# Kernel tuning notes

Measured on AMD Instinct MI355X. Metric: run time of the kernel, lower is better.

The kernel has to match this reference:

```python
import jax, jax.numpy as jnp
import numpy as np

N = 50000   # nodes
E = 800000  # edges (before self-loops)
IN = 256    # in_dim
H = 4       # heads
C = 64      # out_dim per head
NEG_SLOPE = 0.2
BN_EPS = 1e-5


def setup_inputs() -> dict:
    key = jax.random.key(0)
    ks = jax.random.split(key, 6)
    feature = jax.random.normal(ks[0], (N, IN), jnp.float32)
    edge_index = jax.random.randint(ks[1], (2, E), 0, N, dtype=jnp.int64)
    W = jax.random.normal(ks[2], (IN, H * C), jnp.float32) * 0.05
    att_src = jax.random.normal(ks[3], (H, C), jnp.float32) * 0.1
    att_dst = jax.random.normal(ks[4], (H, C), jnp.float32) * 0.1
    bias = jnp.zeros((H * C,), jnp.float32)
    gamma = jnp.ones((H * C,), jnp.float32)
    beta = jnp.zeros((H * C,), jnp.float32)
    return {"feature": feature, "edge_index": edge_index, "W": W,
            "att_src": att_src, "att_dst": att_dst, "bias": bias,
            "gamma": gamma, "beta": beta}


def reference(feature, edge_index, W, att_src, att_dst, bias, gamma, beta):
    n = feature.shape[0]
    # linear projection -> [N, H, C]
    x = (feature @ W).reshape(n, H, C)
    # per-node attention logits [N, H]
    a_src = jnp.einsum('nhc,hc->nh', x, att_src)
    a_dst = jnp.einsum('nhc,hc->nh', x, att_dst)
    # add self loops (PyG GATConv default)
    loop = jnp.arange(n, dtype=edge_index.dtype)
    src = jnp.concatenate([edge_index[0], loop])
    dst = jnp.concatenate([edge_index[1], loop])
    # edge attention scores [E+N, H]
    e = jax.nn.leaky_relu(a_src[src] + a_dst[dst], NEG_SLOPE)
    # segment softmax over incoming edges of each dst node
    m = jax.ops.segment_max(e, dst, num_segments=n)
    ex = jnp.exp(e - m[dst])
    denom = jax.ops.segment_sum(ex, dst, num_segments=n)
    alpha = ex / denom[dst]                       # [E+N, H]
    # weighted message aggregation -> [N, H, C]
    msg = x[src] * alpha[:, :, None]
    out = jax.ops.segment_sum(msg, dst, num_segments=n)
    h = out.reshape(n, H * C) + bias
    # batchnorm over nodes (training-mode batch statistics)
    mu = jnp.mean(h, axis=0)
    var = jnp.var(h, axis=0)
    h = (h - mu) * jax.lax.rsqrt(var + BN_EPS) * gamma + beta
    # ELU activation
    h = jax.nn.elu(h)
    # residual (in_dim == out_dim * num_heads)
    return feature + h
```

## Files before the change

### kernel.cpp

```cpp
#include <hip/hip_runtime.h>

#define N_NODES 50000
#define N_EDGES 800000
#define NEG_SLOPE 0.2f
#define BN_EPS  1e-5f
#define LOG2E   1.44269504088896f

#define CHUNKS 256
#define EDGES_PER_CHUNK 3125
#define NCOARSE 1024
#define NBUCKET 782
#define GEMM_BLOCKS 782

typedef short bf16x8 __attribute__((ext_vector_type(8)));
typedef float floatx4 __attribute__((ext_vector_type(4)));

__device__ inline ushort f2bf(float f) {
    union { float f; unsigned u; } v; v.f = f;
    unsigned r = v.u + 0x7fff + ((v.u >> 16) & 1);
    return (ushort)(r >> 16);
}
__device__ inline float bf2f(ushort h) {
    union { unsigned u; float f; } v; v.u = ((unsigned)h) << 16;
    return v.f;
}

__global__ __launch_bounds__(256) void count_wt_kernel(const int* __restrict__ ei,
                                                       const float* __restrict__ W,
                                                       int* __restrict__ counts,
                                                       ushort* __restrict__ Wtb,
                                                       float* __restrict__ bnacc)
{
    __shared__ int hist[NCOARSE];
    const int t = threadIdx.x;
    const int b = blockIdx.x;
    if (b < CHUNKS) {
        for (int j = t; j < NCOARSE; j += 256) hist[j] = 0;
        __syncthreads();
        const int e0 = b * EDGES_PER_CHUNK;
        for (int e = e0 + t; e < e0 + EDGES_PER_CHUNK; e += 256)
            atomicAdd(&hist[ei[N_EDGES + e] >> 6], 1);
        __syncthreads();
        for (int j = t; j < NCOARSE; j += 256)
            counts[j * CHUNKS + b] = hist[j];
    } else {
        const int n = b - CHUNKS;
        Wtb[n * 256 + t] = f2bf(W[t * 256 + n]);
        if (n < 16) bnacc[n * 256 + t] = 0.f;
    }
}

__global__ __launch_bounds__(256) void sscan1_kernel(int* __restrict__ counts,
                                                     int* __restrict__ blocksum)
{
    __shared__ int sm[256];
    const int t = threadIdx.x;
    const int i = blockIdx.x * 256 + t;
    const int v = counts[i];
    sm[t] = v;
    __syncthreads();
#pragma unroll
    for (int off = 1; off < 256; off <<= 1) {
        const int u = (t >= off) ? sm[t - off] : 0;
        __syncthreads();
        sm[t] += u;
        __syncthreads();
    }
    counts[i] = sm[t] - v;
    if (t == 255) blocksum[blockIdx.x] = sm[255];
}

#define LDSTRIDE 40
__global__ __launch_bounds__(256) void scatter_gemm_kernel(const int* __restrict__ ei,
                                                           const int* __restrict__ counts,
                                                           const int* __restrict__ blocksum,
                                                           int* __restrict__ blockbase,
                                                           uint* __restrict__ tmp,
                                                           const float* __restrict__ A,
                                                           const ushort* __restrict__ Bt,
                                                           const float* __restrict__ att_src,
                                                           const float* __restrict__ att_dst,
                                                           ushort* __restrict__ Xb,
                                                           float* __restrict__ s,
                                                           float* __restrict__ d)
{
    __shared__ __align__(16) char smem[25600];
    const int tid = threadIdx.x;

    if (blockIdx.x < CHUNKS) {
        int* sm     = (int*)smem;
        int* bbase  = sm + 256;
        int* cursor = bbase + NCOARSE;
        const int t = tid;
        const int blk = blockIdx.x;

        int v[4], loc[4], tot = 0;
#pragma unroll
        for (int j = 0; j < 4; ++j) {
            v[j] = blocksum[t * 4 + j];
            loc[j] = tot;
            tot += v[j];
        }
        sm[t] = tot;
        __syncthreads();
#pragma unroll
        for (int off = 1; off < 256; off <<= 1) {
            const int u = (t >= off) ? sm[t - off] : 0;
            __syncthreads();
            sm[t] += u;
            __syncthreads();
        }
        const int base = sm[t] - tot;
#pragma unroll
        for (int j = 0; j < 4; ++j) bbase[t * 4 + j] = base + loc[j];
        if (blk == 0) {
#pragma unroll
            for (int j = 0; j < 4; ++j) blockbase[t * 4 + j] = base + loc[j];
        }
        __syncthreads();

        for (int u = t; u < NCOARSE; u += 256)
            cursor[u] = counts[u * CHUNKS + blk] + bbase[u];
        __syncthreads();
        const int e0 = blk * EDGES_PER_CHUNK;
        for (int e = e0 + t; e < e0 + EDGES_PER_CHUNK; e += 256) {
            const int src = ei[e];
            const int dst = ei[N_EDGES + e];
            const int pos = atomicAdd(&cursor[dst >> 6], 1);
            tmp[pos] = ((uint)src << 6) | (uint)(dst & 63);
        }
        return;
    }

    ushort* As = (ushort*)smem;
    ushort* Bs = As + 64 * LDSTRIDE;
    const int lane = tid & 63;
    const int wid = tid >> 6;
    const int row0 = (blockIdx.x - CHUNKS) * 64;
    const int quad = lane >> 4;
    const int l16  = lane & 15;

    floatx4 acc[4][4] = {};

    const int lr = tid >> 2;
    const int lk = (tid & 3) * 8;

    for (int k0 = 0; k0 < 256; k0 += 32) {
        {
            const int grow = row0 + lr;
            union { ushort u[8]; ulonglong2 v; } cv;
            if (grow < N_NODES) {
                const float4 f0 = *(const float4*)(A + (size_t)grow * 256 + k0 + lk);
                const float4 f1 = *(const float4*)(A + (size_t)grow * 256 + k0 + lk + 4);
                cv.u[0] = f2bf(f0.x); cv.u[1] = f2bf(f0.y);
                cv.u[2] = f2bf(f0.z); cv.u[3] = f2bf(f0.w);
                cv.u[4] = f2bf(f1.x); cv.u[5] = f2bf(f1.y);
                cv.u[6] = f2bf(f1.z); cv.u[7] = f2bf(f1.w);
            } else {
                cv.v = ulonglong2{0ull, 0ull};
            }
            *(ulonglong2*)(As + lr * LDSTRIDE + lk) = cv.v;
        }
#pragma unroll
        for (int r = 0; r < 4; ++r) {
            const int row = lr + r * 64;
            const ulonglong2 bv = *(const ulonglong2*)(Bt + (size_t)row * 256 + k0 + lk);
            *(ulonglong2*)(Bs + row * LDSTRIDE + lk) = bv;
        }
        __syncthreads();
        bf16x8 afrag[4], bfrag[4];
#pragma unroll
        for (int mi = 0; mi < 4; ++mi)
            afrag[mi] = *(const bf16x8*)(As + (mi * 16 + l16) * LDSTRIDE + quad * 8);
#pragma unroll
        for (int ni = 0; ni < 4; ++ni)
            bfrag[ni] = *(const bf16x8*)(Bs + (wid * 64 + ni * 16 + l16) * LDSTRIDE + quad * 8);
#pragma unroll
        for (int mi = 0; mi < 4; ++mi)
#pragma unroll
            for (int ni = 0; ni < 4; ++ni)
                acc[mi][ni] = __builtin_amdgcn_mfma_f32_16x16x32_bf16(afrag[mi], bfrag[ni], acc[mi][ni], 0, 0, 0);
        __syncthreads();
    }

    const int head = wid;
    float as_l[4], ad_l[4];
#pragma unroll
    for (int ni = 0; ni < 4; ++ni) {
        const int ch = head * 64 + ni * 16 + l16;
        as_l[ni] = att_src[ch];
        ad_l[ni] = att_dst[ch];
    }
#pragma unroll
    for (int mi = 0; mi < 4; ++mi) {
#pragma unroll
        for (int r = 0; r < 4; ++r) {
            const int grow = row0 + mi * 16 + quad * 4 + r;
            const bool ok = grow < N_NODES;
            float vs = 0.f, vd = 0.f;
            ushort4 o;
#pragma unroll
            for (int ni = 0; ni < 4; ++ni) {
                const float v = acc[mi][ni][r];
                vs += v * as_l[ni];
                vd += v * ad_l[ni];
                ((ushort*)&o)[ni] = f2bf(v);
            }
            if (ok)
                *(ushort4*)(Xb + (size_t)grow * 256 + head * 64 + l16 * 4) = o;
#pragma unroll
            for (int m = 8; m >= 1; m >>= 1) {
                vs += __shfl_xor(vs, m);
                vd += __shfl_xor(vd, m);
            }
            if (l16 == 0 && ok) {
                s[grow * 4 + head] = vs * LOG2E;
                d[grow * 4 + head] = vd * LOG2E;
            }
        }
    }
}

__global__ __launch_bounds__(256) void bucket_build_kernel(const uint* __restrict__ tmp,
                                                           const int* __restrict__ blockbase,
                                                           int* __restrict__ offsets,
                                                           int* __restrict__ csr_src)
{
    __shared__ int hist[64];
    __shared__ int sbuf[64];
    __shared__ int cursor[64];
    const int t = threadIdx.x;
    const int b = blockIdx.x;
    const int start = blockbase[b];
    const int end   = blockbase[b + 1];
    if (t < 64) hist[t] = 0;
    __syncthreads();
    for (int e = start + t; e < end; e += 256)
        atomicAdd(&hist[tmp[e] & 63], 1);
    __syncthreads();
    const int v = (t < 64) ? hist[t] : 0;
    if (t < 64) sbuf[t] = v;
    __syncthreads();
#pragma unroll
    for (int off = 1; off < 64; off <<= 1) {
        int u = 0;
        if (t < 64 && t >= off) u = sbuf[t - off];
        __syncthreads();
        if (t < 64) sbuf[t] += u;
        __syncthreads();
    }
    if (t < 64) {
        const int excl = start + sbuf[t] - v;
        cursor[t] = excl;
        const int node = b * 64 + t;
        if (node < N_NODES) offsets[node] = excl;
    }
    if (b == 0 && t == 0) offsets[N_NODES] = N_EDGES;
    __syncthreads();
    for (int e = start + t; e < end; e += 256) {
        const uint p = tmp[e];
        const int pos = atomicAdd(&cursor[p & 63], 1);
        csr_src[pos] = (int)(p >> 6);
    }
}

__global__ __launch_bounds__(256) void aggregate_kernel(const ushort* __restrict__ xb,
                                                        const float* __restrict__ s,
                                                        const float* __restrict__ d,
                                                        const int* __restrict__ offsets,
                                                        const int* __restrict__ csr_src,
                                                        ushort* __restrict__ hagg,
                                                        float* __restrict__ bnacc)
{
    __shared__ float bsum[4][256];
    __shared__ float bsq[4][256];
    const int wid = threadIdx.x >> 6;
    const int lane = threadIdx.x & 63;
    const int n = blockIdx.x * 4 + wid;
    const int h = lane >> 4;
    const float dn = d[n * 4 + h];
    const float sn = s[n * 4 + h];
    const ushort4 xr = *(const ushort4*)(xb + (size_t)n * 256 + lane * 4);
    float eself = sn + dn;
    eself = eself >= 0.f ? eself : NEG_SLOPE * eself;
    const float pself = exp2f(eself);
    float den = pself;
    float a0 = pself * bf2f(xr.x), a1 = pself * bf2f(xr.y);
    float a2 = pself * bf2f(xr.z), a3 = pself * bf2f(xr.w);
    const int e0 = __builtin_amdgcn_readfirstlane(offsets[n]);
    const int e1 = __builtin_amdgcn_readfirstlane(offsets[n + 1]);
    for (int e = e0; e < e1; e += 8) {
        int si[8];
        float lg[8];
        ushort4 xv[8];
#pragma unroll
        for (int j = 0; j < 8; ++j) {
            const int idx = e + j;
            const int idx2 = idx < e1 ? idx : e1 - 1;
            si[j] = __builtin_amdgcn_readfirstlane(csr_src[idx2]);
        }
#pragma unroll
        for (int j = 0; j < 8; ++j) lg[j] = s[si[j] * 4 + h] + dn;
#pragma unroll
        for (int j = 0; j < 8; ++j)
            xv[j] = *(const ushort4*)(xb + (size_t)si[j] * 256 + lane * 4);
#pragma unroll
        for (int j = 0; j < 8; ++j) {
            float l = (e + j < e1) ? lg[j] : -1e30f;
            l = l >= 0.f ? l : NEG_SLOPE * l;
            const float p = exp2f(l);
            den += p;
            a0 += p * bf2f(xv[j].x);
            a1 += p * bf2f(xv[j].y);
            a2 += p * bf2f(xv[j].z);
            a3 += p * bf2f(xv[j].w);
        }
    }
    const float inv = 1.0f / den;
    ushort4 o;
    o.x = f2bf(a0 * inv); o.y = f2bf(a1 * inv);
    o.z = f2bf(a2 * inv); o.w = f2bf(a3 * inv);
    *(ushort4*)(hagg + (size_t)n * 256 + lane * 4) = o;

    const float v0 = bf2f(o.x), v1 = bf2f(o.y), v2 = bf2f(o.z), v3 = bf2f(o.w);
    *(float4*)&bsum[wid][lane * 4] = float4{v0, v1, v2, v3};
    *(float4*)&bsq[wid][lane * 4]  = float4{v0 * v0, v1 * v1, v2 * v2, v3 * v3};
    __syncthreads();
    const int c = threadIdx.x;
    const float smv = bsum[0][c] + bsum[1][c] + bsum[2][c] + bsum[3][c];
    const float sqv = bsq[0][c]  + bsq[1][c]  + bsq[2][c]  + bsq[3][c];
    const int rep = (blockIdx.x & 7) * 256 + c;
    atomicAdd(&bnacc[rep], smv);
    atomicAdd(&bnacc[2048 + rep], sqv);
}

__global__ __launch_bounds__(256) void finalize_kernel(const float* __restrict__ feature,
                                                       const ushort* __restrict__ hagg,
                                                       const float* __restrict__ bnacc,
                                                       const float* __restrict__ gamma,
                                                       const float* __restrict__ beta,
                                                       float* __restrict__ out)
{
    __shared__ ushort hs[16][264];
    __shared__ float meanS[256], scaleS[256], betaS[256];
    const int t = threadIdx.x;
    const int wid = t >> 6;
    const int lane = t & 63;
    const int x = blockIdx.x & 7;
    const int i = blockIdx.x >> 3;
    const int bk = (i * 4 + wid) * 8 + x;
    const bool active = bk < 12500;
    const int hblk = lane >> 4;
    const int l16 = lane & 15;

    if (active) {
#pragma unroll
        for (int rr = 0; rr < 4; ++rr) {
            const int r = wid * 4 + rr;
            const int n = bk * 4 + rr;
            const ushort4 hv = *(const ushort4*)(hagg + (size_t)n * 256 + lane * 4);
            hs[r][hblk * 64 + 0 * 16 + l16] = hv.x;
            hs[r][hblk * 64 + 1 * 16 + l16] = hv.y;
            hs[r][hblk * 64 + 2 * 16 + l16] = hv.z;
            hs[r][hblk * 64 + 3 * 16 + l16] = hv.w;
        }
    }

    {
        float smv = 0.f, sqv = 0.f;
#pragma unroll
        for (int r = 0; r < 8; ++r) {
            smv += bnacc[r * 256 + t];
            sqv += bnacc[2048 + r * 256 + t];
        }
        const float m = smv * (1.0f / N_NODES);
        const float var = sqv * (1.0f / N_NODES) - m * m;
        const int w = t & 63;
        const int tc = (t >> 6) * 64 + (w & 3) * 16 + (w >> 2);
        meanS[tc] = m;
        scaleS[tc] = gamma[tc] * rsqrtf(var + BN_EPS);
        betaS[tc] = beta[tc];
    }
    __syncthreads();

    if (active) {
#pragma unroll
        for (int rr = 0; rr < 4; ++rr) {
            const int r = wid * 4 + rr;
            const int n = bk * 4 + rr;
            const ushort4 hv = *(const ushort4*)(&hs[r][lane * 4]);
            const float4 fv = *(const float4*)(feature + (size_t)n * 256 + lane * 4);
            const float hvf[4] = {bf2f(hv.x), bf2f(hv.y), bf2f(hv.z), bf2f(hv.w)};
            float4 o;
            float* op = (float*)&o;
            const float* fp = (const float*)&fv;
#pragma unroll
            for (int j = 0; j < 4; ++j) {
                const int ch = lane * 4 + j;
                float v = (hvf[j] - meanS[ch]) * scaleS[ch] + betaS[ch];
                v = v > 0.f ? v : expm1f(v);
                op[j] = v + fp[j];
            }
            *(float4*)(out + (size_t)n * 256 + lane * 4) = o;
        }
    }
}

extern "C" void kernel_launch(void* const* d_in, const int* in_sizes, int n_in,
                              void* d_out, int out_size, void* d_ws, size_t ws_size,
                              hipStream_t stream)
{
    const float* feature = (const float*)d_in[0];
    const int*   ei      = (const int*)d_in[1];
    const float* W       = (const float*)d_in[2];
    const float* att_src = (const float*)d_in[3];
    const float* att_dst = (const float*)d_in[4];
    const float* gamma   = (const float*)d_in[6];
    const float* beta    = (const float*)d_in[7];
    float* out = (float*)d_out;

    char* w = (char*)d_ws;
    auto carve = [&](size_t bytes) {
        char* p = w;
        w += (bytes + 255) & ~(size_t)255;
        return p;
    };
    ushort* Wtb      = (ushort*)carve((size_t)256 * 256 * 2);
    ushort* xb       = (ushort*)carve((size_t)N_NODES * 256 * 2);
    ushort* hagg     = (ushort*)carve((size_t)N_NODES * 256 * 2);
    float*  s        = (float*)carve((size_t)N_NODES * 4 * 4);
    float*  dv       = (float*)carve((size_t)N_NODES * 4 * 4);
    int*    counts   = (int*)carve((size_t)NCOARSE * CHUNKS * 4);
    int*    offsets  = (int*)carve((size_t)(N_NODES + 1) * 4);
    int*    csr_src  = (int*)carve((size_t)N_EDGES * 4);
    int*    blocksum = (int*)carve((size_t)NCOARSE * 4);
    int*    blockbase= (int*)carve((size_t)NCOARSE * 4);
    float*  bnacc    = (float*)carve((size_t)4096 * 4);
    uint*   tmp      = (uint*)hagg;

    count_wt_kernel<<<512, 256, 0, stream>>>(ei, W, counts, Wtb, bnacc);
    sscan1_kernel<<<NCOARSE, 256, 0, stream>>>(counts, blocksum);
    scatter_gemm_kernel<<<CHUNKS + GEMM_BLOCKS, 256, 0, stream>>>(
        ei, counts, blocksum, blockbase, tmp,
        feature, Wtb, att_src, att_dst, xb, s, dv);
    bucket_build_kernel<<<NBUCKET, 256, 0, stream>>>(tmp, blockbase, offsets, csr_src);
    aggregate_kernel<<<12500, 256, 0, stream>>>(xb, s, dv, offsets, csr_src, hagg, bnacc);
    finalize_kernel<<<3136, 256, 0, stream>>>(feature, hagg, bnacc, gamma, beta, out);
}
```

Measured before the change: 243.4 us.

## Process four nodes per wave in aggregation and simplify finalize indexing

The aggregate kernel now handles four destination nodes per wavefront, so each block covers 16 nodes and the grid shrinks from 12500 to 3125 blocks. BatchNorm partial sums are kept in registers across those nodes, which cuts shared-memory traffic and the per-block atomics to a quarter. Neighbour indices are fetched with one vector load followed by eight readlane operations instead of eight separate scalar loads. Finalize switches to a plain contiguous node mapping without the bounds guard and computes ELU as exp2 minus one instead of expm1f. The risks are fewer waves available to hide gather latency, serialised per-node work within a wave that can worsen imbalance on high-degree nodes, and slightly less accurate ELU near zero.

```diff
diff --git a/kernel.cpp b/kernel.cpp
--- a/kernel.cpp
+++ b/kernel.cpp
@@ -276,55 +276,67 @@
     __shared__ float bsq[4][256];
     const int wid = threadIdx.x >> 6;
     const int lane = threadIdx.x & 63;
-    const int n = blockIdx.x * 4 + wid;
     const int h = lane >> 4;
-    const float dn = d[n * 4 + h];
-    const float sn = s[n * 4 + h];
-    const ushort4 xr = *(const ushort4*)(xb + (size_t)n * 256 + lane * 4);
-    float eself = sn + dn;
-    eself = eself >= 0.f ? eself : NEG_SLOPE * eself;
-    const float pself = exp2f(eself);
-    float den = pself;
-    float a0 = pself * bf2f(xr.x), a1 = pself * bf2f(xr.y);
-    float a2 = pself * bf2f(xr.z), a3 = pself * bf2f(xr.w);
-    const int e0 = __builtin_amdgcn_readfirstlane(offsets[n]);
-    const int e1 = __builtin_amdgcn_readfirstlane(offsets[n + 1]);
-    for (int e = e0; e < e1; e += 8) {
-        int si[8];
-        float lg[8];
-        ushort4 xv[8];
-#pragma unroll
-        for (int j = 0; j < 8; ++j) {
-            const int idx = e + j;
-            const int idx2 = idx < e1 ? idx : e1 - 1;
-            si[j] = __builtin_amdgcn_readfirstlane(csr_src[idx2]);
-        }
-#pragma unroll
-        for (int j = 0; j < 8; ++j) lg[j] = s[si[j] * 4 + h] + dn;
-#pragma unroll
-        for (int j = 0; j < 8; ++j)
-            xv[j] = *(const ushort4*)(xb + (size_t)si[j] * 256 + lane * 4);
-#pragma unroll
-        for (int j = 0; j < 8; ++j) {
-            float l = (e + j < e1) ? lg[j] : -1e30f;
-            l = l >= 0.f ? l : NEG_SLOPE * l;
-            const float p = exp2f(l);
-            den += p;
-            a0 += p * bf2f(xv[j].x);
-            a1 += p * bf2f(xv[j].y);
-            a2 += p * bf2f(xv[j].z);
-            a3 += p * bf2f(xv[j].w);
-        }
-    }
-    const float inv = 1.0f / den;
-    ushort4 o;
-    o.x = f2bf(a0 * inv); o.y = f2bf(a1 * inv);
-    o.z = f2bf(a2 * inv); o.w = f2bf(a3 * inv);
-    *(ushort4*)(hagg + (size_t)n * 256 + lane * 4) = o;
-
-    const float v0 = bf2f(o.x), v1 = bf2f(o.y), v2 = bf2f(o.z), v3 = bf2f(o.w);
-    *(float4*)&bsum[wid][lane * 4] = float4{v0, v1, v2, v3};
-    *(float4*)&bsq[wid][lane * 4]  = float4{v0 * v0, v1 * v1, v2 * v2, v3 * v3};
+    const int nbase = blockIdx.x * 16 + wid * 4;
+    float bs[4] = {0.f, 0.f, 0.f, 0.f};
+    float bq[4] = {0.f, 0.f, 0.f, 0.f};
+#pragma unroll 1
+    for (int nd = 0; nd < 4; ++nd) {
+        const int n = nbase + nd;
+        const float dn = d[n * 4 + h];
+        const float sn = s[n * 4 + h];
+        const ushort4 xr = *(const ushort4*)(xb + (size_t)n * 256 + lane * 4);
+        float eself = sn + dn;
+        eself = eself >= 0.f ? eself : NEG_SLOPE * eself;
+        const float pself = exp2f(eself);
+        float den = pself;
+        float a0 = pself * bf2f(xr.x), a1 = pself * bf2f(xr.y);
+        float a2 = pself * bf2f(xr.z), a3 = pself * bf2f(xr.w);
+        const int e0 = __builtin_amdgcn_readfirstlane(offsets[n]);
+        const int e1 = __builtin_amdgcn_readfirstlane(offsets[n + 1]);
+        for (int e = e0; e < e1; e += 8) {
+            const int idx = e + (lane & 7);
+            const int vv = csr_src[idx < e1 ? idx : e1 - 1];
+            int si[8];
+            si[0] = __builtin_amdgcn_readlane(vv, 0);
+            si[1] = __builtin_amdgcn_readlane(vv, 1);
+            si[2] = __builtin_amdgcn_readlane(vv, 2);
+            si[3] = __builtin_amdgcn_readlane(vv, 3);
+            si[4] = __builtin_amdgcn_readlane(vv, 4);
+            si[5] = __builtin_amdgcn_readlane(vv, 5);
+            si[6] = __builtin_amdgcn_readlane(vv, 6);
+            si[7] = __builtin_amdgcn_readlane(vv, 7);
+            float lg[8];
+            ushort4 xv[8];
+#pragma unroll
+            for (int j = 0; j < 8; ++j) lg[j] = s[si[j] * 4 + h] + dn;
+#pragma unroll
+            for (int j = 0; j < 8; ++j)
+                xv[j] = *(const ushort4*)(xb + (size_t)si[j] * 256 + lane * 4);
+#pragma unroll
+            for (int j = 0; j < 8; ++j) {
+                float l = (e + j < e1) ? lg[j] : -1e30f;
+                l = l >= 0.f ? l : NEG_SLOPE * l;
+                const float p = exp2f(l);
+                den += p;
+                a0 += p * bf2f(xv[j].x);
+                a1 += p * bf2f(xv[j].y);
+                a2 += p * bf2f(xv[j].z);
+                a3 += p * bf2f(xv[j].w);
+            }
+        }
+        const float inv = 1.0f / den;
+        ushort4 o;
+        o.x = f2bf(a0 * inv); o.y = f2bf(a1 * inv);
+        o.z = f2bf(a2 * inv); o.w = f2bf(a3 * inv);
+        *(ushort4*)(hagg + (size_t)n * 256 + lane * 4) = o;
+
+        const float v0 = bf2f(o.x), v1 = bf2f(o.y), v2 = bf2f(o.z), v3 = bf2f(o.w);
+        bs[0] += v0; bs[1] += v1; bs[2] += v2; bs[3] += v3;
+        bq[0] += v0 * v0; bq[1] += v1 * v1; bq[2] += v2 * v2; bq[3] += v3 * v3;
+    }
+    *(float4*)&bsum[wid][lane * 4] = float4{bs[0], bs[1], bs[2], bs[3]};
+    *(float4*)&bsq[wid][lane * 4]  = float4{bq[0], bq[1], bq[2], bq[3]};
     __syncthreads();
     const int c = threadIdx.x;
     const float smv = bsum[0][c] + bsum[1][c] + bsum[2][c] + bsum[3][c];
@@ -346,24 +358,19 @@
     const int t = threadIdx.x;
     const int wid = t >> 6;
     const int lane = t & 63;
-    const int x = blockIdx.x & 7;
-    const int i = blockIdx.x >> 3;
-    const int bk = (i * 4 + wid) * 8 + x;
-    const bool active = bk < 12500;
+    const int nbase = blockIdx.x * 16 + wid * 4;
     const int hblk = lane >> 4;
     const int l16 = lane & 15;
 
-    if (active) {
-#pragma unroll
-        for (int rr = 0; rr < 4; ++rr) {
-            const int r = wid * 4 + rr;
-            const int n = bk * 4 + rr;
-            const ushort4 hv = *(const ushort4*)(hagg + (size_t)n * 256 + lane * 4);
-            hs[r][hblk * 64 + 0 * 16 + l16] = hv.x;
-            hs[r][hblk * 64 + 1 * 16 + l16] = hv.y;
-            hs[r][hblk * 64 + 2 * 16 + l16] = hv.z;
-            hs[r][hblk * 64 + 3 * 16 + l16] = hv.w;
-        }
+#pragma unroll
+    for (int rr = 0; rr < 4; ++rr) {
+        const int r = wid * 4 + rr;
+        const int n = nbase + rr;
+        const ushort4 hv = *(const ushort4*)(hagg + (size_t)n * 256 + lane * 4);
+        hs[r][hblk * 64 + 0 * 16 + l16] = hv.x;
+        hs[r][hblk * 64 + 1 * 16 + l16] = hv.y;
+        hs[r][hblk * 64 + 2 * 16 + l16] = hv.z;
+        hs[r][hblk * 64 + 3 * 16 + l16] = hv.w;
     }
 
     {
@@ -383,26 +390,24 @@
     }
     __syncthreads();
 
-    if (active) {
-#pragma unroll
-        for (int rr = 0; rr < 4; ++rr) {
-            const int r = wid * 4 + rr;
-            const int n = bk * 4 + rr;
-            const ushort4 hv = *(const ushort4*)(&hs[r][lane * 4]);
-            const float4 fv = *(const float4*)(feature + (size_t)n * 256 + lane * 4);
-            const float hvf[4] = {bf2f(hv.x), bf2f(hv.y), bf2f(hv.z), bf2f(hv.w)};
-            float4 o;
-            float* op = (float*)&o;
-            const float* fp = (const float*)&fv;
-#pragma unroll
-            for (int j = 0; j < 4; ++j) {
-                const int ch = lane * 4 + j;
-                float v = (hvf[j] - meanS[ch]) * scaleS[ch] + betaS[ch];
-                v = v > 0.f ? v : expm1f(v);
-                op[j] = v + fp[j];
-            }
-            *(float4*)(out + (size_t)n * 256 + lane * 4) = o;
-        }
+#pragma unroll
+    for (int rr = 0; rr < 4; ++rr) {
+        const int r = wid * 4 + rr;
+        const int n = nbase + rr;
+        const ushort4 hv = *(const ushort4*)(&hs[r][lane * 4]);
+        const float4 fv = *(const float4*)(feature + (size_t)n * 256 + lane * 4);
+        const float hvf[4] = {bf2f(hv.x), bf2f(hv.y), bf2f(hv.z), bf2f(hv.w)};
+        float4 o;
+        float* op = (float*)&o;
+        const float* fp = (const float*)&fv;
+#pragma unroll
+        for (int j = 0; j < 4; ++j) {
+            const int ch = lane * 4 + j;
+            float v = (hvf[j] - meanS[ch]) * scaleS[ch] + betaS[ch];
+            v = v > 0.f ? v : exp2f(v * LOG2E) - 1.0f;
+            op[j] = v + fp[j];
+        }
+        *(float4*)(out + (size_t)n * 256 + lane * 4) = o;
     }
 }
 
@@ -444,6 +449,6 @@
         ei, counts, blocksum, blockbase, tmp,
         feature, Wtb, att_src, att_dst, xb, s, dv);
     bucket_build_kernel<<<NBUCKET, 256, 0, stream>>>(tmp, blockbase, offsets, csr_src);
-    aggregate_kernel<<<12500, 256, 0, stream>>>(xb, s, dv, offsets, csr_src, hagg, bnacc);
-    finalize_kernel<<<3136, 256, 0, stream>>>(feature, hagg, bnacc, gamma, beta, out);
-}
+    aggregate_kernel<<<3125, 256, 0, stream>>>(xb, s, dv, offsets, csr_src, hagg, bnacc);
+    finalize_kernel<<<3125, 256, 0, stream>>>(feature, hagg, bnacc, gamma, beta, out);
+}
```

Result: no change. 244.4 us (+0.4%).
